# Optimization experiments

Hardware: AMD Instinct MI355X
Metric: run time of the kernel (lower is better)

Reference implementation:

```python
import jax, jax.numpy as jnp
import numpy as np

B, T, D = 4, 2048, 1024
E, K = 8, 2
H = int(D * 2.0)  # d_hidden


def setup_inputs() -> dict:
    key = jax.random.key(0)
    ks = jax.random.split(key, 7)
    x = jax.random.normal(ks[0], (B, T, D), dtype=jnp.float32)
    # router Linear(d_model, n_experts)
    router_w = jax.random.normal(ks[1], (D, E), dtype=jnp.float32) * (1.0 / np.sqrt(D))
    router_b = jnp.zeros((E,), dtype=jnp.float32)
    # expert weights, xavier_uniform-like scale
    lim1 = float(np.sqrt(6.0 / (D + H)))
    lim2 = float(np.sqrt(6.0 / (H + D)))
    w1 = jax.random.uniform(ks[2], (E, D, H), dtype=jnp.float32, minval=-lim1, maxval=lim1)
    b1 = jnp.zeros((E, H), dtype=jnp.float32)
    w2 = jax.random.uniform(ks[3], (E, H, D), dtype=jnp.float32, minval=-lim2, maxval=lim2)
    b2 = jnp.zeros((E, D), dtype=jnp.float32)
    return {"x": x, "router_w": router_w, "router_b": router_b,
            "w1": w1, "b1": b1, "w2": w2, "b2": b2}


def reference(x, router_w, router_b, w1, b1, w2, b2):
    Bs, Ts, d = x.shape
    N = Bs * Ts
    h = x.reshape(N, d)
    logits = h @ router_w + router_b                      # [N, E]
    probs = jax.nn.softmax(logits, axis=-1)
    weights, indices = jax.lax.top_k(probs, K)            # [N, K]
    weights = weights / (jnp.sum(weights, axis=-1, keepdims=True) + 1e-9)
    rows = jnp.arange(N)[:, None]
    # routing mask M and combine weights G (scatter over expert axis)
    M = jnp.zeros((N, E), dtype=bool).at[rows, indices].set(True)
    G = jnp.zeros((N, E), dtype=x.dtype).at[rows, indices].add(weights)
    # dense expert compute; tokens with G[:,e]==0 contribute nothing,
    # matching the masked gather/scatter loop exactly (dropout=0, eval mode)
    hidden = jax.nn.gelu(jnp.einsum('nd,edh->enh', h, w1) + b1[:, None, :],
                         approximate=False)               # [E, N, H]
    expert_out = jnp.einsum('enh,ehd->end', hidden, w2) + b2[:, None, :]  # [E, N, D]
    y = jnp.einsum('ne,end->nd', G, expert_out)           # combine
    y = y.reshape(Bs, Ts, d)
    # aux losses
    f_e = M.astype(jnp.float32).mean(axis=0)
    P_e = probs.mean(axis=0)
    lb_loss = -E * jnp.sum(f_e * P_e)
    z = jax.nn.logsumexp(logits, axis=-1)
    z_loss = jnp.mean(z ** 2)
    entropy = jnp.mean(-jnp.sum(probs * jnp.log(probs + 1e-10), axis=-1))
    return (y, lb_loss, z_loss, entropy, f_e, P_e)
```

## Files before the change

kernel.cpp:

```cpp
#include <hip/hip_runtime.h>
#include <hip/hip_bf16.h>

#define NTOK 8192
#define DM 1024
#define NE 8
#define DH 2048
#define CAP 17408
#define NRT 136

typedef __attribute__((ext_vector_type(8))) short short8;
typedef __attribute__((ext_vector_type(4))) float float4v;

#define ASYNC_COPY16(gsrc, ldst)                                                              \
    __builtin_amdgcn_global_load_lds((const __attribute__((address_space(1))) unsigned int*)(gsrc), \
                                     (__attribute__((address_space(3))) unsigned int*)(ldst), \
                                     16, 0, 0)

static __device__ __forceinline__ unsigned short f2bf(float f) {
    __hip_bfloat16 h = __float2bfloat16(f);
    return *reinterpret_cast<unsigned short*>(&h);
}

static __device__ __forceinline__ float fast_gelu(float v) {
    float x = v * 0.70710678118654752f;
    float ax = fabsf(x);
    float t = __frcp_rn(1.0f + 0.3275911f * ax);
    float poly = ((((1.061405429f * t - 1.453152027f) * t + 1.421413741f) * t
                   - 0.284496736f) * t + 0.254829592f) * t;
    float y = 1.0f - poly * __expf(-ax * ax);
    float erfv = copysignf(y, x);
    return 0.5f * v * (1.0f + erfv);
}


__global__ __launch_bounds__(256) void k_transpose(const float* __restrict__ src,
                                                   __hip_bfloat16* __restrict__ dst,
                                                   int R, int C) {
    __shared__ float t[64][65];
    size_t mat = (size_t)blockIdx.z * R * C;
    src += mat;
    dst += mat;
    int c0 = blockIdx.x * 64, r0 = blockIdx.y * 64;
    int tx = threadIdx.x & 63, ty = threadIdx.x >> 6;
#pragma unroll
    for (int i = 0; i < 16; i++) {
        int r = ty + i * 4;
        t[r][tx] = src[(size_t)(r0 + r) * C + c0 + tx];
    }
    __syncthreads();
    int rx = (threadIdx.x & 15) * 4;
    int cy = threadIdx.x >> 4;
#pragma unroll
    for (int i = 0; i < 4; i++) {
        int c = cy + i * 16;
        ushort4 v;
        v.x = f2bf(t[rx + 0][c]);
        v.y = f2bf(t[rx + 1][c]);
        v.z = f2bf(t[rx + 2][c]);
        v.w = f2bf(t[rx + 3][c]);
        *(ushort4*)((unsigned short*)dst + (size_t)(c0 + c) * R + r0 + rx) = v;
    }
}


__global__ __launch_bounds__(256) void k_router(const float* __restrict__ x,
                                                const float* __restrict__ rw,
                                                const float* __restrict__ rb,
                                                __hip_bfloat16* __restrict__ xb,
                                                int* __restrict__ topidx,
                                                float* __restrict__ topw,
                                                float* __restrict__ probs8,
                                                float* __restrict__ zent) {
    int lane = threadIdx.x & 63, wv = threadIdx.x >> 6;
    int n = blockIdx.x * 4 + wv;
    const float* xr = x + (size_t)n * DM;
    unsigned short* xbr = (unsigned short*)xb + (size_t)n * DM;
    float p[8] = {0.f, 0.f, 0.f, 0.f, 0.f, 0.f, 0.f, 0.f};
#pragma unroll
    for (int i = 0; i < 16; i++) {
        int d = lane + i * 64;
        float xv = xr[d];
        xbr[d] = f2bf(xv);
        const float4* w4 = (const float4*)(rw + (size_t)d * 8);
        float4 wa = w4[0], wb = w4[1];
        p[0] += xv * wa.x; p[1] += xv * wa.y; p[2] += xv * wa.z; p[3] += xv * wa.w;
        p[4] += xv * wb.x; p[5] += xv * wb.y; p[6] += xv * wb.z; p[7] += xv * wb.w;
    }
#pragma unroll
    for (int e = 0; e < 8; e++) {
#pragma unroll
        for (int off = 32; off > 0; off >>= 1) p[e] += __shfl_down(p[e], off);
    }
    if (lane == 0) {
        float logits[8], probs[8];
        float mx = -1e30f;
#pragma unroll
        for (int e = 0; e < 8; e++) {
            logits[e] = p[e] + rb[e];
            mx = fmaxf(mx, logits[e]);
        }
        float se = 0.f;
#pragma unroll
        for (int e = 0; e < 8; e++) {
            probs[e] = __expf(logits[e] - mx);
            se += probs[e];
        }
        float inv = 1.f / se;
        float z = mx + logf(se);
        float ent = 0.f;
#pragma unroll
        for (int e = 0; e < 8; e++) {
            probs[e] *= inv;
            ent -= probs[e] * logf(probs[e] + 1e-10f);
        }
        int i0 = 0;
#pragma unroll
        for (int e = 1; e < 8; e++)
            if (probs[e] > probs[i0]) i0 = e;
        int i1 = (i0 == 0) ? 1 : 0;
#pragma unroll
        for (int e = 0; e < 8; e++)
            if (e != i0 && e != i1 && probs[e] > probs[i1]) i1 = e;
        float w0 = probs[i0], w1v = probs[i1];
        float s = w0 + w1v + 1e-9f;
        topidx[2 * n] = i0;
        topidx[2 * n + 1] = i1;
        topw[2 * n] = w0 / s;
        topw[2 * n + 1] = w1v / s;
        float* pr = probs8 + (size_t)n * 8;
#pragma unroll
        for (int e = 0; e < 8; e++) pr[e] = probs[e];
        zent[2 * n] = z * z;
        zent[2 * n + 1] = ent;
    }
}


__global__ __launch_bounds__(256) void k_stats(const int* __restrict__ topidx,
                                               const float* __restrict__ probs8,
                                               const float* __restrict__ zent,
                                               float* __restrict__ fcnt,
                                               float* __restrict__ sump,
                                               float* __restrict__ szent) {
    int n = blockIdx.x * 256 + threadIdx.x;
    float v[18];
    int e0 = topidx[2 * n], e1 = topidx[2 * n + 1];
#pragma unroll
    for (int e = 0; e < 8; e++) v[e] = (float)((e == e0) + (e == e1));
    const float4* p4 = (const float4*)(probs8 + (size_t)n * 8);
    float4 pa = p4[0], pb = p4[1];
    v[8] = pa.x; v[9] = pa.y; v[10] = pa.z; v[11] = pa.w;
    v[12] = pb.x; v[13] = pb.y; v[14] = pb.z; v[15] = pb.w;
    v[16] = zent[2 * n];
    v[17] = zent[2 * n + 1];
#pragma unroll
    for (int i = 0; i < 18; i++)
#pragma unroll
        for (int off = 32; off > 0; off >>= 1) v[i] += __shfl_down(v[i], off);
    __shared__ float part[4][18];
    int lane = threadIdx.x & 63, wv = threadIdx.x >> 6;
    if (lane == 0)
#pragma unroll
        for (int i = 0; i < 18; i++) part[wv][i] = v[i];
    __syncthreads();
    if (threadIdx.x == 0) {
#pragma unroll
        for (int i = 0; i < 18; i++) {
            float s = part[0][i] + part[1][i] + part[2][i] + part[3][i];
            if (i < 8) atomicAdd(&fcnt[i], s);
            else if (i < 16) atomicAdd(&sump[i - 8], s);
            else atomicAdd(&szent[i - 16], s);
        }
    }
}


__global__ void k_scan(const float* __restrict__ fcnt, int* __restrict__ offs) {
    if (threadIdx.x == 0 && blockIdx.x == 0) {
        int o = 0;
        for (int e = 0; e < NE; e++) {
            offs[e] = o;
            int c = (int)(fcnt[e] + 0.5f);
            o += (c + 127) & ~127;
        }
        offs[NE] = o;
    }
}

__global__ __launch_bounds__(256) void k_scatter(const int* __restrict__ topidx,
                                                 const float* __restrict__ topw,
                                                 const int* __restrict__ offs,
                                                 int* __restrict__ cnt2,
                                                 int* __restrict__ rowtok,
                                                 float* __restrict__ roww,
                                                 int* __restrict__ slot) {
    __shared__ int lcnt[8], lbase[8];
    int tid = threadIdx.x;
    if (tid < 8) lcnt[tid] = 0;
    __syncthreads();
    int n = blockIdx.x * 256 + tid;
    int e0 = topidx[2 * n], e1 = topidx[2 * n + 1];
    int p0 = atomicAdd(&lcnt[e0], 1);
    int p1 = atomicAdd(&lcnt[e1], 1);
    __syncthreads();
    if (tid < 8) lbase[tid] = atomicAdd(&cnt2[tid], lcnt[tid]);
    __syncthreads();
    int r0 = offs[e0] + lbase[e0] + p0;
    int r1 = offs[e1] + lbase[e1] + p1;
    rowtok[r0] = n; roww[r0] = topw[2 * n];     slot[2 * n] = r0;
    rowtok[r1] = n; roww[r1] = topw[2 * n + 1]; slot[2 * n + 1] = r1;
}


__global__ __launch_bounds__(256) void k_gemm1(const __hip_bfloat16* __restrict__ xb,
                                               const __hip_bfloat16* __restrict__ w1T,
                                               const float* __restrict__ b1,
                                               const int* __restrict__ rowtok,
                                               const int* __restrict__ offs,
                                               __hip_bfloat16* __restrict__ hid) {
    int bid = blockIdx.x;
    int ib = bid >> 3;
    int row0 = ((bid & 7) * 17 + (ib >> 4)) * 128;
    if (row0 >= offs[NE]) return;
    int h0 = (ib & 15) * 128;
    int e = 0;
    while (row0 >= offs[e + 1]) e++;
    int tid = threadIdx.x;

    __shared__ __align__(16) short A_lds[2][4096];
    __shared__ __align__(16) short B_lds[2][4096];
    __shared__ int tokoff[128];
    if (tid < 128) {
        int t = rowtok[row0 + tid];
        tokoff[tid] = (t < 0 ? 0 : t) * DM;
    }
    __syncthreads();

    int lane = tid & 63, wv = tid >> 6;
    int lr = lane >> 2, pc = lane & 3;
    int ra = wv * 16 + lr;
    int rbr = ra + 64;
    int ch = pc ^ ((ra >> 1) & 3);
    const short* a0 = (const short*)xb + tokoff[ra] + ch * 8;
    const short* a1 = (const short*)xb + tokoff[rbr] + ch * 8;
    const short* bs0 = (const short*)w1T + ((size_t)e * DH + h0 + ra) * DM + ch * 8;
    const short* bs1 = (const short*)w1T + ((size_t)e * DH + h0 + rbr) * DM + ch * 8;
    int ld0 = ra * 32 + pc * 8;
    int ld1 = rbr * 32 + pc * 8;

    int wm = (wv >> 1) * 64, wn = (wv & 1) * 64;
    int quad = lane >> 4, l16 = lane & 15;
    int a_off[4], b_off[4];
#pragma unroll
    for (int t = 0; t < 4; t++) {
        int arow = wm + t * 16 + l16;
        a_off[t] = arow * 32 + ((quad ^ ((arow >> 1) & 3)) * 8);
        int bcol = wn + t * 16 + l16;
        b_off[t] = bcol * 32 + ((quad ^ ((bcol >> 1) & 3)) * 8);
    }
    float4v acc[4][4];
#pragma unroll
    for (int i2 = 0; i2 < 4; i2++)
#pragma unroll
        for (int j = 0; j < 4; j++) {
            float4v z = {0.f, 0.f, 0.f, 0.f};
            acc[i2][j] = z;
        }

    ASYNC_COPY16(a0, &A_lds[0][ld0]);
    ASYNC_COPY16(a1, &A_lds[0][ld1]);
    ASYNC_COPY16(bs0, &B_lds[0][ld0]);
    ASYNC_COPY16(bs1, &B_lds[0][ld1]);
#pragma unroll 1
    for (int it = 0; it < DM / 32; ++it) {
        __syncthreads();
        if (it + 1 < DM / 32) {
            int k0 = (it + 1) * 32, nb = (it + 1) & 1;
            ASYNC_COPY16(a0 + k0, &A_lds[nb][ld0]);
            ASYNC_COPY16(a1 + k0, &A_lds[nb][ld1]);
            ASYNC_COPY16(bs0 + k0, &B_lds[nb][ld0]);
            ASYNC_COPY16(bs1 + k0, &B_lds[nb][ld1]);
        }
        int buf = it & 1;
#pragma unroll
        for (int mt = 0; mt < 4; mt++) {
            short8 a = *(const short8*)&A_lds[buf][a_off[mt]];
#pragma unroll
            for (int nt = 0; nt < 4; nt++) {
                short8 b = *(const short8*)&B_lds[buf][b_off[nt]];
                acc[mt][nt] = __builtin_amdgcn_mfma_f32_16x16x32_bf16(a, b, acc[mt][nt], 0, 0, 0);
            }
        }
    }

    const float* b1e = b1 + (size_t)e * DH + h0;
#pragma unroll
    for (int mt = 0; mt < 4; mt++) {
#pragma unroll
        for (int nt = 0; nt < 4; nt++) {
            int rl = wm + mt * 16 + quad * 4;
            int cl = wn + nt * 16 + l16;
            float bias = b1e[cl];
#pragma unroll
            for (int r = 0; r < 4; r++) {
                float v = fast_gelu(acc[mt][nt][r] + bias);
                hid[(size_t)(row0 + rl + r) * DH + h0 + cl] = __float2bfloat16(v);
            }
        }
    }
}


__global__ __launch_bounds__(256) void k_gemm2(const __hip_bfloat16* __restrict__ hid,
                                               const __hip_bfloat16* __restrict__ w2T,
                                               const float* __restrict__ b2,
                                               const float* __restrict__ roww,
                                               const int* __restrict__ offs,
                                               float* __restrict__ outb) {
    int bid = blockIdx.x;
    int ib = bid >> 3;
    int row0 = ((bid & 7) * 17 + (ib >> 3)) * 128;
    if (row0 >= offs[NE]) return;
    int d0 = (ib & 7) * 128;
    int e = 0;
    while (row0 >= offs[e + 1]) e++;
    int tid = threadIdx.x;

    __shared__ __align__(16) short A_lds[2][4096];
    __shared__ __align__(16) short B_lds[2][4096];

    int lane = tid & 63, wv = tid >> 6;
    int lr = lane >> 2, pc = lane & 3;
    int ra = wv * 16 + lr;
    int rbr = ra + 64;
    int ch = pc ^ ((ra >> 1) & 3);
    const short* a0 = (const short*)hid + (size_t)(row0 + ra) * DH + ch * 8;
    const short* a1 = (const short*)hid + (size_t)(row0 + rbr) * DH + ch * 8;
    const short* bs0 = (const short*)w2T + ((size_t)e * DM + d0 + ra) * DH + ch * 8;
    const short* bs1 = (const short*)w2T + ((size_t)e * DM + d0 + rbr) * DH + ch * 8;
    int ld0 = ra * 32 + pc * 8;
    int ld1 = rbr * 32 + pc * 8;

    int wm = (wv >> 1) * 64, wn = (wv & 1) * 64;
    int quad = lane >> 4, l16 = lane & 15;
    int a_off[4], b_off[4];
#pragma unroll
    for (int t = 0; t < 4; t++) {
        int arow = wm + t * 16 + l16;
        a_off[t] = arow * 32 + ((quad ^ ((arow >> 1) & 3)) * 8);
        int bcol = wn + t * 16 + l16;
        b_off[t] = bcol * 32 + ((quad ^ ((bcol >> 1) & 3)) * 8);
    }
    float4v acc[4][4];
#pragma unroll
    for (int i2 = 0; i2 < 4; i2++)
#pragma unroll
        for (int j = 0; j < 4; j++) {
            float4v z = {0.f, 0.f, 0.f, 0.f};
            acc[i2][j] = z;
        }

    ASYNC_COPY16(a0, &A_lds[0][ld0]);
    ASYNC_COPY16(a1, &A_lds[0][ld1]);
    ASYNC_COPY16(bs0, &B_lds[0][ld0]);
    ASYNC_COPY16(bs1, &B_lds[0][ld1]);
#pragma unroll 1
    for (int it = 0; it < DH / 32; ++it) {
        __syncthreads();
        if (it + 1 < DH / 32) {
            int k0 = (it + 1) * 32, nb = (it + 1) & 1;
            ASYNC_COPY16(a0 + k0, &A_lds[nb][ld0]);
            ASYNC_COPY16(a1 + k0, &A_lds[nb][ld1]);
            ASYNC_COPY16(bs0 + k0, &B_lds[nb][ld0]);
            ASYNC_COPY16(bs1 + k0, &B_lds[nb][ld1]);
        }
        int buf = it & 1;
#pragma unroll
        for (int mt = 0; mt < 4; mt++) {
            short8 a = *(const short8*)&A_lds[buf][a_off[mt]];
#pragma unroll
            for (int nt = 0; nt < 4; nt++) {
                short8 b = *(const short8*)&B_lds[buf][b_off[nt]];
                acc[mt][nt] = __builtin_amdgcn_mfma_f32_16x16x32_bf16(a, b, acc[mt][nt], 0, 0, 0);
            }
        }
    }

    const float* b2e = b2 + (size_t)e * DM + d0;
#pragma unroll
    for (int mt = 0; mt < 4; mt++) {
#pragma unroll
        for (int nt = 0; nt < 4; nt++) {
            int rl = wm + mt * 16 + quad * 4;
            int cl = wn + nt * 16 + l16;
            float bias = b2e[cl];
#pragma unroll
            for (int r = 0; r < 4; r++) {
                int grow = row0 + rl + r;
                float v = (acc[mt][nt][r] + bias) * roww[grow];
                outb[(size_t)grow * DM + d0 + cl] = v;
            }
        }
    }
}


__global__ __launch_bounds__(256) void k_combine(const float* __restrict__ outb,
                                                 const int* __restrict__ slot,
                                                 float* __restrict__ y) {
    int n = blockIdx.x;
    int r0 = slot[2 * n], r1 = slot[2 * n + 1];
    const float4* p0 = (const float4*)(outb + (size_t)r0 * DM);
    const float4* p1 = (const float4*)(outb + (size_t)r1 * DM);
    float4 a = p0[threadIdx.x], b = p1[threadIdx.x];
    float4 c;
    c.x = a.x + b.x;
    c.y = a.y + b.y;
    c.z = a.z + b.z;
    c.w = a.w + b.w;
    ((float4*)(y + (size_t)n * DM))[threadIdx.x] = c;
}

__global__ void k_finalize(const float* __restrict__ fcnt, const float* __restrict__ sump,
                           const float* __restrict__ szent, float* __restrict__ out) {
    if (threadIdx.x == 0 && blockIdx.x == 0) {
        const float invN = 1.0f / (float)NTOK;
        float lb = 0.f;
        float f[NE], P[NE];
        for (int e = 0; e < NE; e++) {
            f[e] = fcnt[e] * invN;
            P[e] = sump[e] * invN;
            lb += f[e] * P[e];
        }
        size_t base = (size_t)NTOK * DM;
        out[base + 0] = -(float)NE * lb;
        out[base + 1] = szent[0] * invN;
        out[base + 2] = szent[1] * invN;
        for (int e = 0; e < NE; e++) out[base + 3 + e] = f[e];
        for (int e = 0; e < NE; e++) out[base + 11 + e] = P[e];
    }
}


extern "C" void kernel_launch(void* const* d_in, const int* in_sizes, int n_in,
                              void* d_out, int out_size, void* d_ws, size_t ws_size,
                              hipStream_t stream) {
    const float* x  = (const float*)d_in[0];
    const float* rw = (const float*)d_in[1];
    const float* rb = (const float*)d_in[2];
    const float* w1 = (const float*)d_in[3];
    const float* b1 = (const float*)d_in[4];
    const float* w2 = (const float*)d_in[5];
    const float* b2 = (const float*)d_in[6];
    float* out = (float*)d_out;

    char* ws = (char*)d_ws;
    size_t o = 0;
    auto alloc = [&](size_t bytes) {
        size_t r = o;
        o = (o + bytes + 255) & ~(size_t)255;
        return r;
    };
    __hip_bfloat16* w1T = (__hip_bfloat16*)(ws + alloc((size_t)NE * DM * DH * 2));
    __hip_bfloat16* w2T = (__hip_bfloat16*)(ws + alloc((size_t)NE * DM * DH * 2));
    __hip_bfloat16* xb  = (__hip_bfloat16*)(ws + alloc((size_t)NTOK * DM * 2));
    __hip_bfloat16* hid = (__hip_bfloat16*)(ws + alloc((size_t)CAP * DH * 2));
    float* outb = (float*)(ws + alloc((size_t)CAP * DM * 4));
    int* rowtok = (int*)(ws + alloc(CAP * 4));
    size_t zstart = o;
    float* roww  = (float*)(ws + alloc(CAP * 4));
    float* fcnt  = (float*)(ws + alloc(64));
    int* cnt2    = (int*)(ws + alloc(64));
    int* offs    = (int*)(ws + alloc(64));
    float* sump  = (float*)(ws + alloc(64));
    float* szent = (float*)(ws + alloc(64));
    size_t zend = o;
    int* topidx = (int*)(ws + alloc((size_t)NTOK * 2 * 4));
    float* topw = (float*)(ws + alloc((size_t)NTOK * 2 * 4));
    int* slot   = (int*)(ws + alloc((size_t)NTOK * 2 * 4));
    float* probs8 = (float*)(ws + alloc((size_t)NTOK * 8 * 4));
    float* zent   = (float*)(ws + alloc((size_t)NTOK * 2 * 4));

    hipMemsetAsync(rowtok, 0xFF, (size_t)CAP * 4, stream);
    hipMemsetAsync(ws + zstart, 0, zend - zstart, stream);

    k_transpose<<<dim3(DH / 64, DM / 64, NE), 256, 0, stream>>>(w1, w1T, DM, DH);
    k_transpose<<<dim3(DM / 64, DH / 64, NE), 256, 0, stream>>>(w2, w2T, DH, DM);
    k_router<<<NTOK / 4, 256, 0, stream>>>(x, rw, rb, xb, topidx, topw, probs8, zent);
    k_stats<<<NTOK / 256, 256, 0, stream>>>(topidx, probs8, zent, fcnt, sump, szent);
    k_scan<<<1, 1, 0, stream>>>(fcnt, offs);
    k_scatter<<<NTOK / 256, 256, 0, stream>>>(topidx, topw, offs, cnt2, rowtok, roww, slot);
    k_gemm1<<<16 * NRT, 256, 0, stream>>>(xb, w1T, b1, rowtok, offs, hid);
    k_gemm2<<<8 * NRT, 256, 0, stream>>>(hid, w2T, b2, roww, offs, outb);
    k_combine<<<NTOK, 256, 0, stream>>>(outb, slot, out);
    k_finalize<<<1, 1, 0, stream>>>(fcnt, sump, szent, out);
}
```

Before: 465.6 us.

## Single-buffer GEMM LDS tiles and store expert outputs as bf16

Both expert GEMM kernels drop LDS double buffering. Each k-step now loads its tile, waits on a barrier, then computes, which halves shared memory per block and may let more blocks run per CU but loses copy/compute overlap. The intermediate per-expert output buffer changes from fp32 to bf16, halving write and read traffic between GEMM2 and the combine kernel. This lowers precision of the weighted expert outputs before they are summed.

```diff
diff --git a/kernel.cpp b/kernel.cpp
--- a/kernel.cpp
+++ b/kernel.cpp
@@ -19,6 +19,11 @@
 static __device__ __forceinline__ unsigned short f2bf(float f) {
     __hip_bfloat16 h = __float2bfloat16(f);
     return *reinterpret_cast<unsigned short*>(&h);
+}
+
+static __device__ __forceinline__ float bf2f(unsigned short u) {
+    unsigned int x = ((unsigned int)u) << 16;
+    return __uint_as_float(x);
 }
 
 static __device__ __forceinline__ float fast_gelu(float v) {
@@ -227,8 +232,8 @@
     while (row0 >= offs[e + 1]) e++;
     int tid = threadIdx.x;
 
-    __shared__ __align__(16) short A_lds[2][4096];
-    __shared__ __align__(16) short B_lds[2][4096];
+    __shared__ __align__(16) short A_lds[4096];
+    __shared__ __align__(16) short B_lds[4096];
     __shared__ int tokoff[128];
     if (tid < 128) {
         int t = rowtok[row0 + tid];
@@ -267,27 +272,21 @@
             acc[i2][j] = z;
         }
 
-    ASYNC_COPY16(a0, &A_lds[0][ld0]);
-    ASYNC_COPY16(a1, &A_lds[0][ld1]);
-    ASYNC_COPY16(bs0, &B_lds[0][ld0]);
-    ASYNC_COPY16(bs1, &B_lds[0][ld1]);
 #pragma unroll 1
     for (int it = 0; it < DM / 32; ++it) {
+        int k0 = it * 32;
         __syncthreads();
-        if (it + 1 < DM / 32) {
-            int k0 = (it + 1) * 32, nb = (it + 1) & 1;
-            ASYNC_COPY16(a0 + k0, &A_lds[nb][ld0]);
-            ASYNC_COPY16(a1 + k0, &A_lds[nb][ld1]);
-            ASYNC_COPY16(bs0 + k0, &B_lds[nb][ld0]);
-            ASYNC_COPY16(bs1 + k0, &B_lds[nb][ld1]);
-        }
-        int buf = it & 1;
+        ASYNC_COPY16(a0 + k0, &A_lds[ld0]);
+        ASYNC_COPY16(a1 + k0, &A_lds[ld1]);
+        ASYNC_COPY16(bs0 + k0, &B_lds[ld0]);
+        ASYNC_COPY16(bs1 + k0, &B_lds[ld1]);
+        __syncthreads();
 #pragma unroll
         for (int mt = 0; mt < 4; mt++) {
-            short8 a = *(const short8*)&A_lds[buf][a_off[mt]];
+            short8 a = *(const short8*)&A_lds[a_off[mt]];
 #pragma unroll
             for (int nt = 0; nt < 4; nt++) {
-                short8 b = *(const short8*)&B_lds[buf][b_off[nt]];
+                short8 b = *(const short8*)&B_lds[b_off[nt]];
                 acc[mt][nt] = __builtin_amdgcn_mfma_f32_16x16x32_bf16(a, b, acc[mt][nt], 0, 0, 0);
             }
         }
@@ -316,7 +315,7 @@
                                                const float* __restrict__ b2,
                                                const float* __restrict__ roww,
                                                const int* __restrict__ offs,
-                                               float* __restrict__ outb) {
+                                               unsigned short* __restrict__ outb) {
     int bid = blockIdx.x;
     int ib = bid >> 3;
     int row0 = ((bid & 7) * 17 + (ib >> 3)) * 128;
@@ -326,8 +325,8 @@
     while (row0 >= offs[e + 1]) e++;
     int tid = threadIdx.x;
 
-    __shared__ __align__(16) short A_lds[2][4096];
-    __shared__ __align__(16) short B_lds[2][4096];
+    __shared__ __align__(16) short A_lds[4096];
+    __shared__ __align__(16) short B_lds[4096];
 
     int lane = tid & 63, wv = tid >> 6;
     int lr = lane >> 2, pc = lane & 3;
@@ -360,27 +359,21 @@
             acc[i2][j] = z;
         }
 
-    ASYNC_COPY16(a0, &A_lds[0][ld0]);
-    ASYNC_COPY16(a1, &A_lds[0][ld1]);
-    ASYNC_COPY16(bs0, &B_lds[0][ld0]);
-    ASYNC_COPY16(bs1, &B_lds[0][ld1]);
 #pragma unroll 1
     for (int it = 0; it < DH / 32; ++it) {
+        int k0 = it * 32;
         __syncthreads();
-        if (it + 1 < DH / 32) {
-            int k0 = (it + 1) * 32, nb = (it + 1) & 1;
-            ASYNC_COPY16(a0 + k0, &A_lds[nb][ld0]);
-            ASYNC_COPY16(a1 + k0, &A_lds[nb][ld1]);
-            ASYNC_COPY16(bs0 + k0, &B_lds[nb][ld0]);
-            ASYNC_COPY16(bs1 + k0, &B_lds[nb][ld1]);
-        }
-        int buf = it & 1;
+        ASYNC_COPY16(a0 + k0, &A_lds[ld0]);
+        ASYNC_COPY16(a1 + k0, &A_lds[ld1]);
+        ASYNC_COPY16(bs0 + k0, &B_lds[ld0]);
+        ASYNC_COPY16(bs1 + k0, &B_lds[ld1]);
+        __syncthreads();
 #pragma unroll
         for (int mt = 0; mt < 4; mt++) {
-            short8 a = *(const short8*)&A_lds[buf][a_off[mt]];
+            short8 a = *(const short8*)&A_lds[a_off[mt]];
 #pragma unroll
             for (int nt = 0; nt < 4; nt++) {
-                short8 b = *(const short8*)&B_lds[buf][b_off[nt]];
+                short8 b = *(const short8*)&B_lds[b_off[nt]];
                 acc[mt][nt] = __builtin_amdgcn_mfma_f32_16x16x32_bf16(a, b, acc[mt][nt], 0, 0, 0);
             }
         }
@@ -398,27 +391,27 @@
             for (int r = 0; r < 4; r++) {
                 int grow = row0 + rl + r;
                 float v = (acc[mt][nt][r] + bias) * roww[grow];
-                outb[(size_t)grow * DM + d0 + cl] = v;
+                outb[(size_t)grow * DM + d0 + cl] = f2bf(v);
             }
         }
     }
 }
 
 
-__global__ __launch_bounds__(256) void k_combine(const float* __restrict__ outb,
+__global__ __launch_bounds__(256) void k_combine(const unsigned short* __restrict__ outb,
                                                  const int* __restrict__ slot,
                                                  float* __restrict__ y) {
     int n = blockIdx.x;
     int r0 = slot[2 * n], r1 = slot[2 * n + 1];
-    const float4* p0 = (const float4*)(outb + (size_t)r0 * DM);
-    const float4* p1 = (const float4*)(outb + (size_t)r1 * DM);
-    float4 a = p0[threadIdx.x], b = p1[threadIdx.x];
-    float4 c;
-    c.x = a.x + b.x;
-    c.y = a.y + b.y;
-    c.z = a.z + b.z;
-    c.w = a.w + b.w;
-    ((float4*)(y + (size_t)n * DM))[threadIdx.x] = c;
+    int c = threadIdx.x * 4;
+    ushort4 a = *(const ushort4*)(outb + (size_t)r0 * DM + c);
+    ushort4 b = *(const ushort4*)(outb + (size_t)r1 * DM + c);
+    float4 o;
+    o.x = bf2f(a.x) + bf2f(b.x);
+    o.y = bf2f(a.y) + bf2f(b.y);
+    o.z = bf2f(a.z) + bf2f(b.z);
+    o.w = bf2f(a.w) + bf2f(b.w);
+    *(float4*)(y + (size_t)n * DM + c) = o;
 }
 
 __global__ void k_finalize(const float* __restrict__ fcnt, const float* __restrict__ sump,
@@ -465,7 +458,7 @@
     __hip_bfloat16* w2T = (__hip_bfloat16*)(ws + alloc((size_t)NE * DM * DH * 2));
     __hip_bfloat16* xb  = (__hip_bfloat16*)(ws + alloc((size_t)NTOK * DM * 2));
     __hip_bfloat16* hid = (__hip_bfloat16*)(ws + alloc((size_t)CAP * DH * 2));
-    float* outb = (float*)(ws + alloc((size_t)CAP * DM * 4));
+    unsigned short* outb = (unsigned short*)(ws + alloc((size_t)CAP * DM * 2));
     int* rowtok = (int*)(ws + alloc(CAP * 4));
     size_t zstart = o;
     float* roww  = (float*)(ws + alloc(CAP * 4));
```

Measured after the change: 500.9 us. 7.6% more time.
